# Performance work log

Measured on AMD Instinct MI355X. Metric: run time of the kernel, lower is better.

The kernel has to match this reference:

```python
import jax, jax.numpy as jnp
import numpy as np

N, D = 8192, 256
NEG_BIG = -9e15


def setup_inputs() -> dict:
    key = jax.random.key(0)
    k1, k2, k3 = jax.random.split(key, 3)
    h = jax.random.normal(k1, (N, D), dtype=jnp.float32)
    adj = jax.random.randint(k2, (N, N), 0, 2, dtype=jnp.int32)
    # xavier_uniform for a of shape (2D, 1): bound = sqrt(6/(2D+1))
    bound = np.sqrt(6.0 / (2 * D + 1)).astype(np.float32)
    a = jax.random.uniform(k3, (2 * D, 1), dtype=jnp.float32, minval=-bound, maxval=bound)
    return {"h": h, "adj": adj, "a": a}


def reference(h, adj, a):
    d = h.shape[1]
    h1 = h @ a[:d]            # [N, 1]
    h2 = h @ a[d:]            # [N, 1]
    e = jax.nn.leaky_relu(h1 + h2.T, negative_slope=0.01)  # [N, N]
    attention = jnp.where(adj > 0, e, NEG_BIG)
    attention = jax.nn.softmax(attention, axis=1)
    # dropout skipped: eval mode (training=False)
    return attention @ h      # [N, D]
```

## Files before the change

### kernel.cpp

```cpp
#include <hip/hip_runtime.h>
#include <hip/hip_bf16.h>

#define NTOT 8192
#define DDIM 256
#define ROWS 32
#define JCHUNK (NTOT / 8)
#define NITER (JCHUNK / 32)
#define NTSTR 131584

typedef __attribute__((ext_vector_type(8))) short short8;
typedef __attribute__((ext_vector_type(4))) float floatx4;
typedef __attribute__((ext_vector_type(4))) int intx4;

__global__ __launch_bounds__(256) void gat_scores(const float* __restrict__ h,
                                                  const float* __restrict__ a,
                                                  float4* __restrict__ rc,
                                                  float2* __restrict__ etab) {
  int row  = blockIdx.x * 4 + (threadIdx.x >> 6);
  int lane = threadIdx.x & 63;
  const float* hr = h + (size_t)row * DDIM;
  float p1 = 0.f, p2 = 0.f;
#pragma unroll
  for (int k = 0; k < DDIM / 64; ++k) {
    int idx  = lane + 64 * k;
    float hv = hr[idx];
    p1 += hv * a[idx];
    p2 += hv * a[DDIM + idx];
  }
#pragma unroll
  for (int off = 32; off > 0; off >>= 1) {
    p1 += __shfl_down(p1, off, 64);
    p2 += __shfl_down(p2, off, 64);
  }
  if (lane == 0) {
    rc[row]   = make_float4(__expf(p1), __expf(0.01f * p1), 0.f, 0.f);
    etab[row] = make_float2(__expf(p2), __expf(0.01f * p2));
  }
}

__global__ __launch_bounds__(256) void gat_hpack(const float* __restrict__ h,
                                                 ushort* __restrict__ hTf) {
  __shared__ float tile[64][257];
  const int t    = threadIdx.x;
  const int lane = t & 63;
  const int w    = t >> 6;
  const int quad = lane >> 4;
  const int c    = lane & 15;
  const int i0   = blockIdx.x * 64;

#pragma unroll
  for (int it = 0; it < 16; ++it) {
    int r = it * 4 + w;
    float4 v = *(const float4*)(h + (size_t)(i0 + r) * DDIM + lane * 4);
    tile[r][lane * 4 + 0] = v.x; tile[r][lane * 4 + 1] = v.y;
    tile[r][lane * 4 + 2] = v.z; tile[r][lane * 4 + 3] = v.w;
  }
  __syncthreads();

#pragma unroll
  for (int k = 0; k < 4; ++k) {
    const int n = 4 * k + w;
#pragma unroll
    for (int jbl = 0; jbl < 2; ++jbl) {
      short8 vv;
#pragma unroll
      for (int i = 0; i < 8; ++i) {
        float f = tile[jbl * 32 + quad * 8 + i][n * 16 + c];
        __hip_bfloat16 b = __float2bfloat16(f);
        vv[i] = *(short*)&b;
      }
      *(short8*)(hTf + ((size_t)(n * 257 + i0 / 32 + jbl) * 64 + lane) * 8) = vv;
    }
  }
}

__global__ __launch_bounds__(512, 2) void gat_attn(const ushort* __restrict__ hTf,
                                                   const int* __restrict__ adj,
                                                   const float4* __restrict__ rc,
                                                   const float2* __restrict__ etab,
                                                   float* __restrict__ out) {
  __shared__ union {
    float lred[8][32];
    float slab[4][ROWS * 128];
  } sh;

  const int t    = threadIdx.x;
  const int lane = t & 63;
  const int w    = t >> 6;
  const int quad = lane >> 4;
  const int c    = lane & 15;
  const int r0   = blockIdx.x * ROWS;

  const float4 rc0 = rc[r0 + c];
  const float4 rc1 = rc[r0 + 16 + c];
  const float E10 = rc0.x, E20 = rc0.y;
  const float E11 = rc1.x, E21 = rc1.y;

  const int* ap0 = adj + (size_t)(r0 + c) * NTOT + (size_t)w * JCHUNK + quad * 8;
  const int* ap1 = ap0 + (size_t)16 * NTOT;
  const float*    etb = (const float*)(etab + (size_t)w * JCHUNK + quad * 8);
  const ushort*   hfp = hTf + ((size_t)(w * 32) * 64 + lane) * 8;

  floatx4 acc[2][16];
#pragma unroll
  for (int rt = 0; rt < 2; ++rt)
#pragma unroll
    for (int nt = 0; nt < 16; ++nt) acc[rt][nt] = (floatx4){0.f, 0.f, 0.f, 0.f};

  float lp0 = 0.f, lp1 = 0.f;
  short8 bA[8], bB[8];

  #define LDH(dst, jt, half)                                                   \
    _Pragma("unroll")                                                          \
    for (int q = 0; q < 8; ++q)                                                \
      dst[q] = *(const short8*)(hfp + (size_t)(jt) * 512 +                     \
                                (size_t)((half) * 8 + q) * NTSTR);

  LDH(bA, 0, 0)
  intx4 A0a = __builtin_nontemporal_load((const intx4*)ap0);
  intx4 A0b = __builtin_nontemporal_load((const intx4*)(ap0 + 4));
  intx4 A1a = __builtin_nontemporal_load((const intx4*)ap1);
  intx4 A1b = __builtin_nontemporal_load((const intx4*)(ap1 + 4));
  float4 ea = ((const float4*)etb)[0];
  float4 eb = ((const float4*)etb)[1];
  float4 ec = ((const float4*)etb)[2];
  float4 ed = ((const float4*)etb)[3];

  for (int jt = 0; jt < NITER; ++jt) {
    const int jn = (jt + 1) & (NITER - 1);

    LDH(bB, jt, 1)

    const int am0[8] = {A0a[0], A0a[1], A0a[2], A0a[3], A0b[0], A0b[1], A0b[2], A0b[3]};
    const int am1[8] = {A1a[0], A1a[1], A1a[2], A1a[3], A1b[0], A1b[1], A1b[2], A1b[3]};
    float tp[16] = {ea.x, ea.y, ea.z, ea.w, eb.x, eb.y, eb.z, eb.w,
                    ec.x, ec.y, ec.z, ec.w, ed.x, ed.y, ed.z, ed.w};
    short8 pa0, pa1;
#pragma unroll
    for (int i = 0; i < 8; ++i) {
      const float t1 = tp[2 * i], t2 = tp[2 * i + 1];
      float p0 = (am0[i] > 0) ? fmaxf(E10 * t1, E20 * t2) : 0.f;
      float p1 = (am1[i] > 0) ? fmaxf(E11 * t1, E21 * t2) : 0.f;
      lp0 += p0; lp1 += p1;
      __hip_bfloat16 b0 = __float2bfloat16(p0);
      __hip_bfloat16 b1 = __float2bfloat16(p1);
      pa0[i] = *(short*)&b0;
      pa1[i] = *(short*)&b1;
    }

    {
      const int* n0 = ap0 + (size_t)jn * 32;
      A0a = __builtin_nontemporal_load((const intx4*)n0);
      A0b = __builtin_nontemporal_load((const intx4*)(n0 + 4));
      const int* n1 = ap1 + (size_t)jn * 32;
      A1a = __builtin_nontemporal_load((const intx4*)n1);
      A1b = __builtin_nontemporal_load((const intx4*)(n1 + 4));
      const float* en = etb + (size_t)jn * 64;
      ea = ((const float4*)en)[0];
      eb = ((const float4*)en)[1];
      ec = ((const float4*)en)[2];
      ed = ((const float4*)en)[3];
    }

#pragma unroll
    for (int q = 0; q < 8; ++q) {
      acc[0][q] = __builtin_amdgcn_mfma_f32_16x16x32_bf16(pa0, bA[q], acc[0][q], 0, 0, 0);
      acc[1][q] = __builtin_amdgcn_mfma_f32_16x16x32_bf16(pa1, bA[q], acc[1][q], 0, 0, 0);
    }
    LDH(bA, jn, 0)

#pragma unroll
    for (int q = 0; q < 8; ++q) {
      acc[0][8 + q] = __builtin_amdgcn_mfma_f32_16x16x32_bf16(pa0, bB[q], acc[0][8 + q], 0, 0, 0);
      acc[1][8 + q] = __builtin_amdgcn_mfma_f32_16x16x32_bf16(pa1, bB[q], acc[1][8 + q], 0, 0, 0);
    }
  }
  #undef LDH

  lp0 += __shfl_xor(lp0, 16, 64); lp0 += __shfl_xor(lp0, 32, 64);
  lp1 += __shfl_xor(lp1, 16, 64); lp1 += __shfl_xor(lp1, 32, 64);
  if (quad == 0) { sh.lred[w][c] = lp0; sh.lred[w][16 + c] = lp1; }
  __syncthreads();

  float linv[2][4];
  if (w == 0) {
#pragma unroll
    for (int rt = 0; rt < 2; ++rt)
#pragma unroll
      for (int reg = 0; reg < 4; ++reg) {
        int lrow = rt * 16 + quad * 4 + reg;
        float s = 0.f;
#pragma unroll
        for (int wi = 0; wi < 8; ++wi) s += sh.lred[wi][lrow];
        linv[rt][reg] = 1.f / s;
      }
  }
  __syncthreads();

#pragma unroll
  for (int hd = 0; hd < 2; ++hd) {
    if (w >= 4) {
#pragma unroll
      for (int rt = 0; rt < 2; ++rt)
#pragma unroll
        for (int i = 0; i < 8; ++i)
#pragma unroll
          for (int reg = 0; reg < 4; ++reg)
            sh.slab[w - 4][(rt * 16 + quad * 4 + reg) * 128 + i * 16 + c] =
                acc[rt][i + 8 * hd][reg];
    }
    __syncthreads();
    if (w < 4) {
#pragma unroll
      for (int rt = 0; rt < 2; ++rt)
#pragma unroll
        for (int i = 0; i < 8; ++i)
#pragma unroll
          for (int reg = 0; reg < 4; ++reg)
            acc[rt][i + 8 * hd][reg] +=
                sh.slab[w][(rt * 16 + quad * 4 + reg) * 128 + i * 16 + c];
    }
    __syncthreads();
    if (w == 2 || w == 3) {
#pragma unroll
      for (int rt = 0; rt < 2; ++rt)
#pragma unroll
        for (int i = 0; i < 8; ++i)
#pragma unroll
          for (int reg = 0; reg < 4; ++reg)
            sh.slab[w - 2][(rt * 16 + quad * 4 + reg) * 128 + i * 16 + c] =
                acc[rt][i + 8 * hd][reg];
    }
    __syncthreads();
    if (w < 2) {
#pragma unroll
      for (int rt = 0; rt < 2; ++rt)
#pragma unroll
        for (int i = 0; i < 8; ++i)
#pragma unroll
          for (int reg = 0; reg < 4; ++reg)
            acc[rt][i + 8 * hd][reg] +=
                sh.slab[w][(rt * 16 + quad * 4 + reg) * 128 + i * 16 + c];
    }
    __syncthreads();
    if (w == 1) {
#pragma unroll
      for (int rt = 0; rt < 2; ++rt)
#pragma unroll
        for (int i = 0; i < 8; ++i)
#pragma unroll
          for (int reg = 0; reg < 4; ++reg)
            sh.slab[0][(rt * 16 + quad * 4 + reg) * 128 + i * 16 + c] =
                acc[rt][i + 8 * hd][reg];
    }
    __syncthreads();
    if (w == 0) {
#pragma unroll
      for (int rt = 0; rt < 2; ++rt)
#pragma unroll
        for (int i = 0; i < 8; ++i)
#pragma unroll
          for (int reg = 0; reg < 4; ++reg) {
            float v = acc[rt][i + 8 * hd][reg] +
                      sh.slab[0][(rt * 16 + quad * 4 + reg) * 128 + i * 16 + c];
            __builtin_nontemporal_store(
                v * linv[rt][reg],
                &out[(size_t)(r0 + rt * 16 + quad * 4 + reg) * DDIM +
                     hd * 128 + i * 16 + c]);
          }
    }
    __syncthreads();
  }
}

extern "C" void kernel_launch(void* const* d_in, const int* in_sizes, int n_in,
                              void* d_out, int out_size, void* d_ws, size_t ws_size,
                              hipStream_t stream) {
  const float* h   = (const float*)d_in[0];
  const int*   adj = (const int*)d_in[1];
  const float* a   = (const float*)d_in[2];
  float* out = (float*)d_out;

  float4*   rc    = (float4*)d_ws;
  float2*   etab  = (float2*)(rc + NTOT);
  ushort*   hTf   = (ushort*)(etab + NTOT);

  gat_scores<<<NTOT / 4, 256, 0, stream>>>(h, a, rc, etab);
  gat_hpack<<<NTOT / 64, 256, 0, stream>>>(h, hTf);
  gat_attn<<<NTOT / ROWS, 512, 0, stream>>>(hTf, adj, rc, etab, out);
}
```

Before: 425.7 us.

## Split attention over two column halves and add a combine kernel

The attention kernel now runs on a 2D grid that divides the key dimension into two halves, doubling the block count from 256 to 512. Each half writes unnormalised partial outputs and partial row sums to workspace, and a new combine kernel adds them and normalises. The bB prefetch is also moved to the end of the loop so the next iteration's loads are issued earlier. This buys more parallelism and better CU occupancy on a 256-CU part, at the cost of writing and re-reading two fp32 partial buffers (about 16 MB) plus an extra launch.

```diff
diff --git a/kernel.cpp b/kernel.cpp
--- a/kernel.cpp
+++ b/kernel.cpp
@@ -4,9 +4,12 @@
 #define NTOT 8192
 #define DDIM 256
 #define ROWS 32
-#define JCHUNK (NTOT / 8)
+#define JSPL 2
+#define JHALF (NTOT / JSPL)
+#define JCHUNK (JHALF / 8)
 #define NITER (JCHUNK / 32)
 #define NTSTR 131584
+#define HTF_ELEMS (16 * NTSTR)
 
 typedef __attribute__((ext_vector_type(8))) short short8;
 typedef __attribute__((ext_vector_type(4))) float floatx4;
@@ -78,7 +81,8 @@
                                                    const int* __restrict__ adj,
                                                    const float4* __restrict__ rc,
                                                    const float2* __restrict__ etab,
-                                                   float* __restrict__ out) {
+                                                   float* __restrict__ pout,
+                                                   float* __restrict__ plp) {
   __shared__ union {
     float lred[8][32];
     float slab[4][ROWS * 128];
@@ -90,16 +94,18 @@
   const int quad = lane >> 4;
   const int c    = lane & 15;
   const int r0   = blockIdx.x * ROWS;
+  const int jb   = blockIdx.y;
+  const int jbase = jb * JHALF;
 
   const float4 rc0 = rc[r0 + c];
   const float4 rc1 = rc[r0 + 16 + c];
   const float E10 = rc0.x, E20 = rc0.y;
   const float E11 = rc1.x, E21 = rc1.y;
 
-  const int* ap0 = adj + (size_t)(r0 + c) * NTOT + (size_t)w * JCHUNK + quad * 8;
+  const int* ap0 = adj + (size_t)(r0 + c) * NTOT + jbase + (size_t)w * JCHUNK + quad * 8;
   const int* ap1 = ap0 + (size_t)16 * NTOT;
-  const float*    etb = (const float*)(etab + (size_t)w * JCHUNK + quad * 8);
-  const ushort*   hfp = hTf + ((size_t)(w * 32) * 64 + lane) * 8;
+  const float*  etb = (const float*)(etab + (size_t)jbase + (size_t)w * JCHUNK + quad * 8);
+  const ushort* hfp = hTf + (size_t)(jbase / 32 + w * (JCHUNK / 32)) * 512 + lane * 8;
 
   floatx4 acc[2][16];
 #pragma unroll
@@ -117,6 +123,7 @@
                                 (size_t)((half) * 8 + q) * NTSTR);
 
   LDH(bA, 0, 0)
+  LDH(bB, 0, 1)
   intx4 A0a = __builtin_nontemporal_load((const intx4*)ap0);
   intx4 A0b = __builtin_nontemporal_load((const intx4*)(ap0 + 4));
   intx4 A1a = __builtin_nontemporal_load((const intx4*)ap1);
@@ -128,8 +135,6 @@
 
   for (int jt = 0; jt < NITER; ++jt) {
     const int jn = (jt + 1) & (NITER - 1);
-
-    LDH(bB, jt, 1)
 
     const int am0[8] = {A0a[0], A0a[1], A0a[2], A0a[3], A0b[0], A0b[1], A0b[2], A0b[3]};
     const int am1[8] = {A1a[0], A1a[1], A1a[2], A1a[3], A1b[0], A1b[1], A1b[2], A1b[3]};
@@ -174,6 +179,7 @@
       acc[0][8 + q] = __builtin_amdgcn_mfma_f32_16x16x32_bf16(pa0, bB[q], acc[0][8 + q], 0, 0, 0);
       acc[1][8 + q] = __builtin_amdgcn_mfma_f32_16x16x32_bf16(pa1, bB[q], acc[1][8 + q], 0, 0, 0);
     }
+    LDH(bB, jn, 1)
   }
   #undef LDH
 
@@ -182,7 +188,6 @@
   if (quad == 0) { sh.lred[w][c] = lp0; sh.lred[w][16 + c] = lp1; }
   __syncthreads();
 
-  float linv[2][4];
   if (w == 0) {
 #pragma unroll
     for (int rt = 0; rt < 2; ++rt)
@@ -192,11 +197,12 @@
         float s = 0.f;
 #pragma unroll
         for (int wi = 0; wi < 8; ++wi) s += sh.lred[wi][lrow];
-        linv[rt][reg] = 1.f / s;
+        if (c == 0) plp[(size_t)jb * NTOT + r0 + lrow] = s;
       }
   }
   __syncthreads();
 
+  float* pob = pout + (size_t)jb * NTOT * DDIM;
 #pragma unroll
   for (int hd = 0; hd < 2; ++hd) {
     if (w >= 4) {
@@ -263,14 +269,31 @@
           for (int reg = 0; reg < 4; ++reg) {
             float v = acc[rt][i + 8 * hd][reg] +
                       sh.slab[0][(rt * 16 + quad * 4 + reg) * 128 + i * 16 + c];
-            __builtin_nontemporal_store(
-                v * linv[rt][reg],
-                &out[(size_t)(r0 + rt * 16 + quad * 4 + reg) * DDIM +
-                     hd * 128 + i * 16 + c]);
+            pob[(size_t)(r0 + rt * 16 + quad * 4 + reg) * DDIM +
+                hd * 128 + i * 16 + c] = v;
           }
     }
     __syncthreads();
   }
+}
+
+__global__ __launch_bounds__(256) void gat_combine(const float* __restrict__ pout,
+                                                   const float* __restrict__ plp,
+                                                   float* __restrict__ out) {
+  const int idx = blockIdx.x * 256 + threadIdx.x;
+  const int row = idx >> 6;
+  float4 a = ((const float4*)pout)[idx];
+  float4 b = ((const float4*)(pout + (size_t)NTOT * DDIM))[idx];
+  float inv = 1.f / (plp[row] + plp[NTOT + row]);
+  float4 r;
+  r.x = (a.x + b.x) * inv;
+  r.y = (a.y + b.y) * inv;
+  r.z = (a.z + b.z) * inv;
+  r.w = (a.w + b.w) * inv;
+  __builtin_nontemporal_store(r.x, &((float*)out)[idx * 4 + 0]);
+  __builtin_nontemporal_store(r.y, &((float*)out)[idx * 4 + 1]);
+  __builtin_nontemporal_store(r.z, &((float*)out)[idx * 4 + 2]);
+  __builtin_nontemporal_store(r.w, &((float*)out)[idx * 4 + 3]);
 }
 
 extern "C" void kernel_launch(void* const* d_in, const int* in_sizes, int n_in,
@@ -284,8 +307,11 @@
   float4*   rc    = (float4*)d_ws;
   float2*   etab  = (float2*)(rc + NTOT);
   ushort*   hTf   = (ushort*)(etab + NTOT);
+  float*    pout  = (float*)(hTf + HTF_ELEMS);
+  float*    plp   = pout + (size_t)JSPL * NTOT * DDIM;
 
   gat_scores<<<NTOT / 4, 256, 0, stream>>>(h, a, rc, etab);
   gat_hpack<<<NTOT / 64, 256, 0, stream>>>(h, hTf);
-  gat_attn<<<NTOT / ROWS, 512, 0, stream>>>(hTf, adj, rc, etab, out);
-}
+  gat_attn<<<dim3(NTOT / ROWS, JSPL), 512, 0, stream>>>(hTf, adj, rc, etab, pout, plp);
+  gat_combine<<<(NTOT * DDIM / 4) / 256, 256, 0, stream>>>(pout, plp, out);
+}
```

New measurement: 438.1 us. 2.9% more time.
